# Optimization experiments

Hardware: AMD Instinct MI355X
Metric: run time of the kernel (lower is better)

Reference implementation:

```python
import jax, jax.numpy as jnp
import numpy as np

N = 50000   # nodes
E = 1600000 # edges
NF = 128    # input features
H = 128     # hidden
C = 40      # classes
EPS = 1e-5


def setup_inputs() -> dict:
    key = jax.random.key(0)
    ks = jax.random.split(key, 8)
    s_in = 1.0 / np.sqrt(NF)
    s_h = 1.0 / np.sqrt(H)
    return {
        "x": jax.random.normal(ks[0], (N, NF), jnp.float32),
        "edge_index": jax.random.randint(ks[1], (2, E), 0, N, dtype=jnp.int32),
        "W1": jax.random.normal(ks[2], (NF, H), jnp.float32) * s_in,
        "b1": jnp.zeros((H,), jnp.float32),
        "W2": jax.random.normal(ks[3], (H, H), jnp.float32) * s_h,
        "b2": jnp.zeros((H,), jnp.float32),
        "W3": jax.random.normal(ks[4], (H, H), jnp.float32) * s_h,
        "b3": jnp.zeros((H,), jnp.float32),
        "g1": jnp.ones((H,), jnp.float32), "be1": jnp.zeros((H,), jnp.float32),
        "g2": jnp.ones((H,), jnp.float32), "be2": jnp.zeros((H,), jnp.float32),
        "g3": jnp.ones((H,), jnp.float32), "be3": jnp.zeros((H,), jnp.float32),
        "fcW": jax.random.normal(ks[5], (H, C), jnp.float32) * s_h,
        "fcb": jnp.zeros((C,), jnp.float32),
    }


def _bn(x, g, b):
    # BatchNorm1d training-mode semantics: batch mean / biased batch var
    m = jnp.mean(x, axis=0)
    v = jnp.mean(jnp.square(x - m), axis=0)
    return g * (x - m) * jax.lax.rsqrt(v + EPS) + b


def reference(x, edge_index, W1, b1, W2, b2, W3, b3,
              g1, be1, g2, be2, g3, be3, fcW, fcb):
    n = x.shape[0]
    loop = jnp.arange(n, dtype=edge_index.dtype)
    src = jnp.concatenate([edge_index[0], loop])  # [E+N]
    dst = jnp.concatenate([edge_index[1], loop])
    # symmetric GCN normalization with self-loops
    deg = jax.ops.segment_sum(jnp.ones_like(src, dtype=x.dtype), dst, num_segments=n)
    dis = jnp.where(deg > 0, jax.lax.rsqrt(jnp.maximum(deg, 1.0)), 0.0)
    norm = dis[src] * dis[dst]  # [E+N]

    def conv(h, W, b):
        hw = h @ W  # [n, H]
        msg = hw[src] * norm[:, None]  # [E+N, H] gather + scale
        return jax.ops.segment_sum(msg, dst, num_segments=n) + b  # scatter-add

    h = jax.nn.relu(_bn(conv(x, W1, b1), g1, be1))
    h = jax.nn.relu(_bn(conv(h, W2, b2), g2, be2))  # dropout: eval mode (identity)
    h = jax.nn.relu(_bn(conv(h, W3, b3), g3, be3))
    logits = jax.nn.relu(h @ fcW + fcb)
    return jax.nn.log_softmax(logits, axis=1), logits
```

## Files before the change

kernel.cpp:

```cpp
#include <hip/hip_runtime.h>
#include <hip/hip_bf16.h>
#include <math.h>

#define NODES 50000
#define EDGES 1600000
#define HD    128
#define NC    40
#define EPSV  1e-5f
#define NBKT  196
#define CSRMAX 12032
#define NPART 32

typedef unsigned int uint;
typedef unsigned short ushort;
typedef __attribute__((ext_vector_type(8))) short bfrag;
typedef __attribute__((ext_vector_type(4))) float ffrag;

union FragU { uint4 u; bfrag f; };

__device__ inline ushort bf1(float x) {
  uint u = __float_as_uint(x);
  return (ushort)((u + 0x7fffu + ((u >> 16) & 1u)) >> 16);
}
__device__ inline uint bf2(float a, float b) {
  return (uint)bf1(a) | ((uint)bf1(b) << 16);
}
__device__ inline float ulo(uint u) { return __uint_as_float(u << 16); }
__device__ inline float uhi(uint u) { return __uint_as_float(u & 0xffff0000u); }


__global__ __launch_bounds__(256)
void k_bcount_prepw(const int* __restrict__ dst, int* __restrict__ bcnt, int e_,
                    const float* __restrict__ W1, const float* __restrict__ W2,
                    const float* __restrict__ W3, const float* __restrict__ fcW,
                    ushort* __restrict__ wt) {
  if (blockIdx.x >= 196) {
    int idx = (blockIdx.x - 196) * 256 + threadIdx.x;
    if (idx < 49152) {
      int r = idx >> 14;
      int i = idx & 16383;
      int nn = i >> 7, k = i & 127;
      const float* W = (r == 0) ? W1 : ((r == 1) ? W2 : W3);
      wt[idx] = bf1(W[k * 128 + nn]);
    } else if (idx < 55296) {
      int i = idx - 49152;
      int nn = i >> 7, k = i & 127;
      wt[idx] = (nn < NC) ? bf1(fcW[k * NC + nn]) : (ushort)0;
    }
    return;
  }
  __shared__ int h[256];
  int t = threadIdx.x;
  h[t] = 0;
  __syncthreads();
  int base = blockIdx.x * 8192;
  int cntE = min(8192, e_ - base);
  for (int i = t; i < cntE; i += 256) atomicAdd(&h[dst[base + i] >> 8], 1);
  __syncthreads();
  if (h[t]) atomicAdd(&bcnt[t], h[t]);
}

__global__ void k_bscan(const int* __restrict__ bcnt, int* __restrict__ bbase,
                        int* __restrict__ bcur, int* __restrict__ row_ptr) {
  __shared__ int s[256];
  int t = threadIdx.x;
  int v = bcnt[t];
  s[t] = v;
  __syncthreads();
#pragma unroll
  for (int off = 1; off < 256; off <<= 1) {
    int y = (t >= off) ? s[t - off] : 0;
    __syncthreads();
    s[t] += y;
    __syncthreads();
  }
  int excl = s[t] - v;
  bbase[t] = excl;
  bcur[t] = excl;
  if (t == 255) {
    bbase[256] = s[255];
    row_ptr[NODES] = s[255];
  }
}

__global__ __launch_bounds__(256)
void k_bin(const int* __restrict__ src, const int* __restrict__ dst,
           int* __restrict__ bcur, uint* __restrict__ staging, int e_) {
  __shared__ uint ent[8192];
  __shared__ int h[256], inc[256], lofs[256], cur[256], gb[256];
  int t = threadIdx.x;
  h[t] = 0;
  __syncthreads();
  int base = blockIdx.x * 8192;
  int cntE = min(8192, e_ - base);
  for (int i = t; i < cntE; i += 256) atomicAdd(&h[dst[base + i] >> 8], 1);
  __syncthreads();
  inc[t] = h[t];
  __syncthreads();
#pragma unroll
  for (int off = 1; off < 256; off <<= 1) {
    int y = (t >= off) ? inc[t - off] : 0;
    __syncthreads();
    inc[t] += y;
    __syncthreads();
  }
  lofs[t] = inc[t] - h[t];
  cur[t] = 0;
  __syncthreads();
  for (int i = t; i < cntE; i += 256) {
    int e = base + i;
    int d = dst[e];
    int b = d >> 8;
    uint en = (uint)(src[e] & 0xffff) | ((uint)(d & 255) << 16) | ((uint)b << 24);
    int p = lofs[b] + atomicAdd(&cur[b], 1);
    ent[p] = en;
  }
  __syncthreads();
  if (h[t]) gb[t] = atomicAdd(&bcur[t], h[t]);
  __syncthreads();
  for (int i = t; i < cntE; i += 256) {
    uint en = ent[i];
    int b = en >> 24;
    staging[gb[b] + (i - lofs[b])] = en;
  }
}

__global__ __launch_bounds__(256)
void k_csr(const uint* __restrict__ staging, const int* __restrict__ bbase,
           ushort* __restrict__ csr, int* __restrict__ row_ptr,
           float* __restrict__ dis, int n) {
  __shared__ uint ent[CSRMAX];
  __shared__ ushort srt[CSRMAX];
  __shared__ int cnt_[256], ofs_[256], cur_[256];
  int b = blockIdx.x, t = threadIdx.x;
  int base = bbase[b];
  int cnt = bbase[b + 1] - base;
  if (cnt > CSRMAX) cnt = CSRMAX;
  for (int i = t; i < cnt; i += 256) ent[i] = staging[base + i];
  cnt_[t] = 0;
  __syncthreads();
  for (int i = t; i < cnt; i += 256) atomicAdd(&cnt_[(ent[i] >> 16) & 255], 1);
  __syncthreads();
  ofs_[t] = cnt_[t];
  __syncthreads();
#pragma unroll
  for (int off = 1; off < 256; off <<= 1) {
    int y = (t >= off) ? ofs_[t - off] : 0;
    __syncthreads();
    ofs_[t] += y;
    __syncthreads();
  }
  int myofs = ofs_[t] - cnt_[t];
  ofs_[t] = myofs;
  cur_[t] = 0;
  __syncthreads();
  int node = (b << 8) + t;
  if (node < n) {
    row_ptr[node] = base + myofs;
    dis[node] = rsqrtf((float)(cnt_[t] + 1));
  }
  for (int i = t; i < cnt; i += 256) {
    uint e = ent[i];
    int dl = (e >> 16) & 255;
    int p = ofs_[dl] + atomicAdd(&cur_[dl], 1);
    srt[p] = (ushort)(e & 0xffff);
  }
  __syncthreads();
  for (int i = t; i < cnt; i += 256) csr[base + i] = srt[i];
}

__global__ __launch_bounds__(256)
void k_wfill(const ushort* __restrict__ csr, const int* __restrict__ row_ptr,
             const float* __restrict__ dis, uint* __restrict__ csrw, int n) {
  int node = blockIdx.x * 4 + (threadIdx.x >> 6);
  if (node >= n) return;
  int lane = threadIdx.x & 63;
  int e0 = row_ptr[node], e1 = row_ptr[node + 1];
  float dd = dis[node];
  for (int e = e0 + lane; e < e1; e += 64) {
    int s = csr[e];
    float w = dis[s] * dd;
    csrw[e] = (uint)s | ((uint)bf1(w) << 16);
  }
}

__device__ inline void bn_prologue(const float* __restrict__ part,
                                   const float* __restrict__ g,
                                   const float* __restrict__ be,
                                   float* s_scale, float* s_shift) {
  __shared__ float tmp[256];
  int t = threadIdx.x;
  float s = 0.f;
#pragma unroll 8
  for (int p = 0; p < NPART; ++p) s += part[p * 256 + t];
  tmp[t] = s;
  __syncthreads();
  if (t < 128) {
    const float inv_n = 1.0f / (float)NODES;
    float m = tmp[t] * inv_n;
    float var = tmp[128 + t] * inv_n - m * m;
    float rstd = rsqrtf(var + EPSV);
    float sc = g[t] * rstd;
    s_scale[t] = sc;
    s_shift[t] = be[t] - m * sc;
  }
  __syncthreads();
}

template<int MODE>
__global__ __launch_bounds__(256)
void k_gemm_mx(const void* __restrict__ Ain, const uint* __restrict__ Wt,
               ushort* __restrict__ Cb, int n,
               const float* __restrict__ part, const float* __restrict__ g,
               const float* __restrict__ be) {
  __shared__ float s_scale[128], s_shift[128];
  if (MODE == 1) bn_prologue(part, g, be, s_scale, s_shift);

  const int lane = threadIdx.x & 63;
  const int wave = threadIdx.x >> 6;
  const int quad = lane >> 4;
  const int ml = lane & 15;
  const int row0 = blockIdx.x * 64 + wave * 16;
  const int arow = row0 + ml;
  ffrag acc[8];
#pragma unroll
  for (int i = 0; i < 8; ++i) acc[i] = (ffrag){0.f, 0.f, 0.f, 0.f};

#pragma unroll
  for (int s = 0; s < 4; ++s) {
    const int k0 = s * 32 + quad * 8;
    FragU a;
    if (arow < n) {
      if (MODE == 1) {
        const uint* Ab = (const uint*)Ain;
        uint4 v = *(const uint4*)&Ab[(size_t)arow * 64 + (k0 >> 1)];
        float4 sc0 = *(const float4*)&s_scale[k0];
        float4 sc1 = *(const float4*)&s_scale[k0 + 4];
        float4 sh0 = *(const float4*)&s_shift[k0];
        float4 sh1 = *(const float4*)&s_shift[k0 + 4];
        a.u.x = bf2(fmaxf(fmaf(ulo(v.x), sc0.x, sh0.x), 0.f), fmaxf(fmaf(uhi(v.x), sc0.y, sh0.y), 0.f));
        a.u.y = bf2(fmaxf(fmaf(ulo(v.y), sc0.z, sh0.z), 0.f), fmaxf(fmaf(uhi(v.y), sc0.w, sh0.w), 0.f));
        a.u.z = bf2(fmaxf(fmaf(ulo(v.z), sc1.x, sh1.x), 0.f), fmaxf(fmaf(uhi(v.z), sc1.y, sh1.y), 0.f));
        a.u.w = bf2(fmaxf(fmaf(ulo(v.w), sc1.z, sh1.z), 0.f), fmaxf(fmaf(uhi(v.w), sc1.w, sh1.w), 0.f));
      } else {
        const float* Af = (const float*)Ain;
        float4 a0 = *(const float4*)&Af[(size_t)arow * 128 + k0];
        float4 a1 = *(const float4*)&Af[(size_t)arow * 128 + k0 + 4];
        a.u.x = bf2(a0.x, a0.y);
        a.u.y = bf2(a0.z, a0.w);
        a.u.z = bf2(a1.x, a1.y);
        a.u.w = bf2(a1.z, a1.w);
      }
    } else {
      a.u = make_uint4(0, 0, 0, 0);
    }
#pragma unroll
    for (int nt = 0; nt < 8; ++nt) {
      FragU b;
      b.u = *(const uint4*)&Wt[(size_t)(nt * 16 + ml) * 64 + (k0 >> 1)];
      acc[nt] = __builtin_amdgcn_mfma_f32_16x16x32_bf16(a.f, b.f, acc[nt], 0, 0, 0);
    }
  }
#pragma unroll
  for (int nt = 0; nt < 8; ++nt) {
#pragma unroll
    for (int r = 0; r < 4; ++r) {
      int orow = row0 + quad * 4 + r;
      if (orow < n) Cb[(size_t)orow * 128 + nt * 16 + ml] = bf1(acc[nt][r]);
    }
  }
}

__global__ __launch_bounds__(256)
void k_agg(const uint* __restrict__ t, const int* __restrict__ row_ptr,
           const uint* __restrict__ csrw, const float* __restrict__ dis,
           uint* __restrict__ hb, float* __restrict__ part, int n) {
  __shared__ float redS[4][128], redQ[4][128];
  int lane = threadIdx.x & 63;
  int wave = threadIdx.x >> 6;
  int quarter = lane >> 4;
  int fl = lane & 15;
  int node0 = blockIdx.x * 16 + wave * 4;
  float sS[8] = {}, sQ[8] = {};

  for (int ni = 0; ni < 4; ++ni) {
    int node = node0 + ni;
    int e0 = row_ptr[node], e1 = row_ptr[node + 1];
    float acc[8] = {};
    for (int chunk = e0; chunk < e1; chunk += 64) {
      int m = min(64, e1 - chunk);
      uint ev = 0;
      if (lane < m) ev = csrw[chunk + lane];
#pragma unroll 2
      for (int j = 0; j < m; j += 8) {
        int j0 = j + quarter, j1 = j + 4 + quarter;
        uint ev0 = __shfl(ev, j0, 64);
        uint ev1 = __shfl(ev, j1, 64);
        bool p0 = j0 < m, p1 = j1 < m;
        uint4 v0 = make_uint4(0, 0, 0, 0), v1 = make_uint4(0, 0, 0, 0);
        if (p0) v0 = *(const uint4*)&t[(size_t)(ev0 & 0xffffu) * 64 + (fl << 2)];
        if (p1) v1 = *(const uint4*)&t[(size_t)(ev1 & 0xffffu) * 64 + (fl << 2)];
        float w0 = __uint_as_float(ev0 & 0xffff0000u);
        float w1 = __uint_as_float(ev1 & 0xffff0000u);
        if (p0) {
          acc[0] = fmaf(w0, ulo(v0.x), acc[0]);
          acc[1] = fmaf(w0, uhi(v0.x), acc[1]);
          acc[2] = fmaf(w0, ulo(v0.y), acc[2]);
          acc[3] = fmaf(w0, uhi(v0.y), acc[3]);
          acc[4] = fmaf(w0, ulo(v0.z), acc[4]);
          acc[5] = fmaf(w0, uhi(v0.z), acc[5]);
          acc[6] = fmaf(w0, ulo(v0.w), acc[6]);
          acc[7] = fmaf(w0, uhi(v0.w), acc[7]);
        }
        if (p1) {
          acc[0] = fmaf(w1, ulo(v1.x), acc[0]);
          acc[1] = fmaf(w1, uhi(v1.x), acc[1]);
          acc[2] = fmaf(w1, ulo(v1.y), acc[2]);
          acc[3] = fmaf(w1, uhi(v1.y), acc[3]);
          acc[4] = fmaf(w1, ulo(v1.z), acc[4]);
          acc[5] = fmaf(w1, uhi(v1.z), acc[5]);
          acc[6] = fmaf(w1, ulo(v1.w), acc[6]);
          acc[7] = fmaf(w1, uhi(v1.w), acc[7]);
        }
      }
    }
#pragma unroll
    for (int j = 0; j < 8; ++j) {
      acc[j] += __shfl_xor(acc[j], 16, 64);
      acc[j] += __shfl_xor(acc[j], 32, 64);
    }
    if (quarter == 0) {
      float dd = dis[node];
      float d2 = dd * dd;
      uint4 v = *(const uint4*)&t[(size_t)node * 64 + (fl << 2)];
      acc[0] = fmaf(d2, ulo(v.x), acc[0]);
      acc[1] = fmaf(d2, uhi(v.x), acc[1]);
      acc[2] = fmaf(d2, ulo(v.y), acc[2]);
      acc[3] = fmaf(d2, uhi(v.y), acc[3]);
      acc[4] = fmaf(d2, ulo(v.z), acc[4]);
      acc[5] = fmaf(d2, uhi(v.z), acc[5]);
      acc[6] = fmaf(d2, ulo(v.w), acc[6]);
      acc[7] = fmaf(d2, uhi(v.w), acc[7]);
      uint4 o;
      o.x = bf2(acc[0], acc[1]);
      o.y = bf2(acc[2], acc[3]);
      o.z = bf2(acc[4], acc[5]);
      o.w = bf2(acc[6], acc[7]);
      *(uint4*)&hb[(size_t)node * 64 + (fl << 2)] = o;
#pragma unroll
      for (int j = 0; j < 8; ++j) {
        sS[j] += acc[j];
        sQ[j] += acc[j] * acc[j];
      }
    }
  }
  if (quarter == 0) {
#pragma unroll
    for (int j = 0; j < 8; ++j) {
      redS[wave][fl * 8 + j] = sS[j];
      redQ[wave][fl * 8 + j] = sQ[j];
    }
  }
  __syncthreads();
  int tt = threadIdx.x;
  if (tt < 128) {
    float s = redS[0][tt] + redS[1][tt] + redS[2][tt] + redS[3][tt];
    atomicAdd(&part[(blockIdx.x & (NPART - 1)) * 256 + tt], s);
  } else {
    int f = tt - 128;
    float s = redQ[0][f] + redQ[1][f] + redQ[2][f] + redQ[3][f];
    atomicAdd(&part[(blockIdx.x & (NPART - 1)) * 256 + tt], s);
  }
}

__global__ __launch_bounds__(256)
void k_fc_mx(const uint* __restrict__ hb, const float* __restrict__ part,
             const float* __restrict__ g, const float* __restrict__ be,
             const uint* __restrict__ fWt, const float* __restrict__ fcb,
             float* __restrict__ out, int n) {
  __shared__ float s_scale[128], s_shift[128];
  bn_prologue(part, g, be, s_scale, s_shift);

  const int lane = threadIdx.x & 63;
  const int wave = threadIdx.x >> 6;
  const int quad = lane >> 4;
  const int ml = lane & 15;
  const int row0 = blockIdx.x * 64 + wave * 16;
  const int arow = row0 + ml;
  ffrag acc[3];
#pragma unroll
  for (int i = 0; i < 3; ++i) acc[i] = (ffrag){0.f, 0.f, 0.f, 0.f};

#pragma unroll
  for (int s = 0; s < 4; ++s) {
    const int k0 = s * 32 + quad * 8;
    FragU a;
    if (arow < n) {
      uint4 v = *(const uint4*)&hb[(size_t)arow * 64 + (k0 >> 1)];
      float4 sc0 = *(const float4*)&s_scale[k0];
      float4 sc1 = *(const float4*)&s_scale[k0 + 4];
      float4 sh0 = *(const float4*)&s_shift[k0];
      float4 sh1 = *(const float4*)&s_shift[k0 + 4];
      a.u.x = bf2(fmaxf(fmaf(ulo(v.x), sc0.x, sh0.x), 0.f), fmaxf(fmaf(uhi(v.x), sc0.y, sh0.y), 0.f));
      a.u.y = bf2(fmaxf(fmaf(ulo(v.y), sc0.z, sh0.z), 0.f), fmaxf(fmaf(uhi(v.y), sc0.w, sh0.w), 0.f));
      a.u.z = bf2(fmaxf(fmaf(ulo(v.z), sc1.x, sh1.x), 0.f), fmaxf(fmaf(uhi(v.z), sc1.y, sh1.y), 0.f));
      a.u.w = bf2(fmaxf(fmaf(ulo(v.w), sc1.z, sh1.z), 0.f), fmaxf(fmaf(uhi(v.w), sc1.w, sh1.w), 0.f));
    } else {
      a.u = make_uint4(0, 0, 0, 0);
    }
#pragma unroll
    for (int nt = 0; nt < 3; ++nt) {
      FragU b;
      b.u = *(const uint4*)&fWt[(size_t)(nt * 16 + ml) * 64 + (k0 >> 1)];
      acc[nt] = __builtin_amdgcn_mfma_f32_16x16x32_bf16(a.f, b.f, acc[nt], 0, 0, 0);
    }
  }

  float b0 = fcb[ml], b1 = fcb[16 + ml];
  float b2 = (ml < 8) ? fcb[32 + ml] : 0.f;
#pragma unroll
  for (int r = 0; r < 4; ++r) {
    int orow = row0 + quad * 4 + r;
    if (orow >= n) continue;
    float l0 = fmaxf(acc[0][r] + b0, 0.f);
    float l1 = fmaxf(acc[1][r] + b1, 0.f);
    float l2 = (ml < 8) ? fmaxf(acc[2][r] + b2, 0.f) : -1e30f;
    float mx = fmaxf(fmaxf(l0, l1), l2);
#pragma unroll
    for (int off = 1; off < 16; off <<= 1) mx = fmaxf(mx, __shfl_xor(mx, off, 64));
    float sm = __expf(l0 - mx) + __expf(l1 - mx) + ((ml < 8) ? __expf(l2 - mx) : 0.f);
#pragma unroll
    for (int off = 1; off < 16; off <<= 1) sm += __shfl_xor(sm, off, 64);
    float lse = mx + __logf(sm);
    float* o1 = out + (size_t)orow * NC;
    float* o2 = out + (size_t)NODES * NC + (size_t)orow * NC;
    o1[ml] = l0 - lse;
    o1[16 + ml] = l1 - lse;
    o2[ml] = l0;
    o2[16 + ml] = l1;
    if (ml < 8) {
      o1[32 + ml] = l2 - lse;
      o2[32 + ml] = l2;
    }
  }
}


extern "C" void kernel_launch(void* const* d_in, const int* in_sizes, int n_in,
                              void* d_out, int out_size, void* d_ws, size_t ws_size,
                              hipStream_t stream) {
  (void)in_sizes; (void)n_in; (void)out_size; (void)ws_size;
  const float* x   = (const float*)d_in[0];
  const int*   ei  = (const int*)d_in[1];
  const float* W1  = (const float*)d_in[2];
  const float* W2  = (const float*)d_in[4];
  const float* W3  = (const float*)d_in[6];
  const float* g1  = (const float*)d_in[8];
  const float* be1 = (const float*)d_in[9];
  const float* g2  = (const float*)d_in[10];
  const float* be2 = (const float*)d_in[11];
  const float* g3  = (const float*)d_in[12];
  const float* be3 = (const float*)d_in[13];
  const float* fcW = (const float*)d_in[14];
  const float* fcb = (const float*)d_in[15];
  float* out = (float*)d_out;

  const int n = NODES, e_ = EDGES;
  const int* srcp = ei;
  const int* dstp = ei + e_;

  char* ws = (char*)d_ws;
  size_t off = 0;
  auto alloc = [&](size_t bytes) {
    char* p = ws + off;
    off = (off + bytes + 255) & ~(size_t)255;
    return p;
  };
  float* dis    = (float*)alloc((size_t)n * 4);
  int*   bcnt   = (int*)  alloc(256 * 4);
  float* parts  = (float*)alloc(3 * NPART * 256 * 4);
  int*   bbase  = (int*)  alloc(257 * 4);
  int*   bcur   = (int*)  alloc(256 * 4);
  int*   row_ptr= (int*)  alloc((size_t)(n + 1) * 4);
  uint*  staging= (uint*) alloc((size_t)e_ * 4);
  ushort* csr   = (ushort*)alloc((size_t)e_ * 2);
  uint*  csrw   = (uint*) alloc((size_t)e_ * 4);
  uint*  tbuf   = (uint*) alloc((size_t)n * 64 * 4);
  uint*  hbuf   = (uint*) alloc((size_t)n * 64 * 4);
  ushort* wbuf  = (ushort*)alloc(55296 * 2);

  const uint* Wt1  = (const uint*)wbuf;
  const uint* Wt2  = (const uint*)wbuf + 8192;
  const uint* Wt3  = (const uint*)wbuf + 16384;
  const uint* fWt  = (const uint*)wbuf + 24576;

  const int ebk = (e_ + 8191) / 8192;

  hipMemsetAsync(bcnt, 0, 256 * 4 + 3 * NPART * 256 * 4, stream);
  k_bcount_prepw<<<ebk + 216, 256, 0, stream>>>(dstp, bcnt, e_, W1, W2, W3, fcW, wbuf);
  k_bscan<<<1, 256, 0, stream>>>(bcnt, bbase, bcur, row_ptr);
  k_bin<<<ebk, 256, 0, stream>>>(srcp, dstp, bcur, staging, e_);
  k_csr<<<NBKT, 256, 0, stream>>>(staging, bbase, csr, row_ptr, dis, n);
  k_wfill<<<n / 4, 256, 0, stream>>>(csr, row_ptr, dis, csrw, n);

  const int ggrid = (n + 63) / 64;
  const int agrid = n / 16;
  float* p0 = parts;
  float* p1 = parts + NPART * 256;
  float* p2 = parts + 2 * NPART * 256;

  k_gemm_mx<0><<<ggrid, 256, 0, stream>>>(x, Wt1, (ushort*)tbuf, n, nullptr, nullptr, nullptr);
  k_agg<<<agrid, 256, 0, stream>>>(tbuf, row_ptr, csrw, dis, hbuf, p0, n);
  k_gemm_mx<1><<<ggrid, 256, 0, stream>>>(hbuf, Wt2, (ushort*)tbuf, n, p0, g1, be1);
  k_agg<<<agrid, 256, 0, stream>>>(tbuf, row_ptr, csrw, dis, hbuf, p1, n);
  k_gemm_mx<1><<<ggrid, 256, 0, stream>>>(hbuf, Wt3, (ushort*)tbuf, n, p1, g2, be2);
  k_agg<<<agrid, 256, 0, stream>>>(tbuf, row_ptr, csrw, dis, hbuf, p2, n);
  k_fc_mx<<<ggrid, 256, 0, stream>>>(hbuf, p2, g3, be3, fWt, fcb, out, n);
}
```

Before: 400.8 us.

## Drop bucket count/scan passes using fixed-capacity buckets and fuse edge-weight fill into first aggregation

Removes the bucket-count and scan kernels by giving each destination bucket a fixed CSRMAX-sized slot in staging, with bcur acting as a per-bucket fill counter. Row pointers become (start,end) pairs inside padded buckets. The separate weight-fill kernel is folded into the first aggregation, which computes and stores the packed index/weight pairs for later layers. The gather loop is also unrolled to four edges per step. This cuts launches and a full pass over the edges, at the cost of padded memory and an assumption that no bucket exceeds CSRMAX edges.

```diff
diff --git a/kernel.cpp b/kernel.cpp
--- a/kernel.cpp
+++ b/kernel.cpp
@@ -28,12 +28,12 @@
 __device__ inline float ulo(uint u) { return __uint_as_float(u << 16); }
 __device__ inline float uhi(uint u) { return __uint_as_float(u & 0xffff0000u); }
 
-
 __global__ __launch_bounds__(256)
-void k_bcount_prepw(const int* __restrict__ dst, int* __restrict__ bcnt, int e_,
-                    const float* __restrict__ W1, const float* __restrict__ W2,
-                    const float* __restrict__ W3, const float* __restrict__ fcW,
-                    ushort* __restrict__ wt) {
+void k_bin_prepw(const int* __restrict__ src, const int* __restrict__ dst,
+                 int* __restrict__ bcur, uint* __restrict__ staging, int e_,
+                 const float* __restrict__ W1, const float* __restrict__ W2,
+                 const float* __restrict__ W3, const float* __restrict__ fcW,
+                 ushort* __restrict__ wt) {
   if (blockIdx.x >= 196) {
     int idx = (blockIdx.x - 196) * 256 + threadIdx.x;
     if (idx < 49152) {
@@ -49,43 +49,6 @@
     }
     return;
   }
-  __shared__ int h[256];
-  int t = threadIdx.x;
-  h[t] = 0;
-  __syncthreads();
-  int base = blockIdx.x * 8192;
-  int cntE = min(8192, e_ - base);
-  for (int i = t; i < cntE; i += 256) atomicAdd(&h[dst[base + i] >> 8], 1);
-  __syncthreads();
-  if (h[t]) atomicAdd(&bcnt[t], h[t]);
-}
-
-__global__ void k_bscan(const int* __restrict__ bcnt, int* __restrict__ bbase,
-                        int* __restrict__ bcur, int* __restrict__ row_ptr) {
-  __shared__ int s[256];
-  int t = threadIdx.x;
-  int v = bcnt[t];
-  s[t] = v;
-  __syncthreads();
-#pragma unroll
-  for (int off = 1; off < 256; off <<= 1) {
-    int y = (t >= off) ? s[t - off] : 0;
-    __syncthreads();
-    s[t] += y;
-    __syncthreads();
-  }
-  int excl = s[t] - v;
-  bbase[t] = excl;
-  bcur[t] = excl;
-  if (t == 255) {
-    bbase[256] = s[255];
-    row_ptr[NODES] = s[255];
-  }
-}
-
-__global__ __launch_bounds__(256)
-void k_bin(const int* __restrict__ src, const int* __restrict__ dst,
-           int* __restrict__ bcur, uint* __restrict__ staging, int e_) {
   __shared__ uint ent[8192];
   __shared__ int h[256], inc[256], lofs[256], cur[256], gb[256];
   int t = threadIdx.x;
@@ -121,21 +84,20 @@
   for (int i = t; i < cntE; i += 256) {
     uint en = ent[i];
     int b = en >> 24;
-    staging[gb[b] + (i - lofs[b])] = en;
+    staging[(size_t)b * CSRMAX + gb[b] + (i - lofs[b])] = en;
   }
 }
 
 __global__ __launch_bounds__(256)
-void k_csr(const uint* __restrict__ staging, const int* __restrict__ bbase,
-           ushort* __restrict__ csr, int* __restrict__ row_ptr,
+void k_csr(const uint* __restrict__ staging, const int* __restrict__ bcur,
+           ushort* __restrict__ csr, int2* __restrict__ row_se,
            float* __restrict__ dis, int n) {
   __shared__ uint ent[CSRMAX];
   __shared__ ushort srt[CSRMAX];
   __shared__ int cnt_[256], ofs_[256], cur_[256];
   int b = blockIdx.x, t = threadIdx.x;
-  int base = bbase[b];
-  int cnt = bbase[b + 1] - base;
-  if (cnt > CSRMAX) cnt = CSRMAX;
+  size_t base = (size_t)b * CSRMAX;
+  int cnt = min(bcur[b], CSRMAX);
   for (int i = t; i < cnt; i += 256) ent[i] = staging[base + i];
   cnt_[t] = 0;
   __syncthreads();
@@ -156,7 +118,7 @@
   __syncthreads();
   int node = (b << 8) + t;
   if (node < n) {
-    row_ptr[node] = base + myofs;
+    row_se[node] = make_int2((int)base + myofs, (int)base + myofs + cnt_[t]);
     dis[node] = rsqrtf((float)(cnt_[t] + 1));
   }
   for (int i = t; i < cnt; i += 256) {
@@ -167,21 +129,6 @@
   }
   __syncthreads();
   for (int i = t; i < cnt; i += 256) csr[base + i] = srt[i];
-}
-
-__global__ __launch_bounds__(256)
-void k_wfill(const ushort* __restrict__ csr, const int* __restrict__ row_ptr,
-             const float* __restrict__ dis, uint* __restrict__ csrw, int n) {
-  int node = blockIdx.x * 4 + (threadIdx.x >> 6);
-  if (node >= n) return;
-  int lane = threadIdx.x & 63;
-  int e0 = row_ptr[node], e1 = row_ptr[node + 1];
-  float dd = dis[node];
-  for (int e = e0 + lane; e < e1; e += 64) {
-    int s = csr[e];
-    float w = dis[s] * dd;
-    csrw[e] = (uint)s | ((uint)bf1(w) << 16);
-  }
 }
 
 __device__ inline void bn_prologue(const float* __restrict__ part,
@@ -271,9 +218,11 @@
   }
 }
 
+template<int FIRST>
 __global__ __launch_bounds__(256)
-void k_agg(const uint* __restrict__ t, const int* __restrict__ row_ptr,
-           const uint* __restrict__ csrw, const float* __restrict__ dis,
+void k_agg(const uint* __restrict__ t, const int2* __restrict__ row_se,
+           const ushort* __restrict__ csr, uint* __restrict__ csrw,
+           const float* __restrict__ dis,
            uint* __restrict__ hb, float* __restrict__ part, int n) {
   __shared__ float redS[4][128], redQ[4][128];
   int lane = threadIdx.x & 63;
@@ -285,42 +234,63 @@
 
   for (int ni = 0; ni < 4; ++ni) {
     int node = node0 + ni;
-    int e0 = row_ptr[node], e1 = row_ptr[node + 1];
+    int2 se = row_se[node];
+    int e0 = se.x, e1 = se.y;
+    float dd = dis[node];
     float acc[8] = {};
     for (int chunk = e0; chunk < e1; chunk += 64) {
       int m = min(64, e1 - chunk);
       uint ev = 0;
-      if (lane < m) ev = csrw[chunk + lane];
-#pragma unroll 2
-      for (int j = 0; j < m; j += 8) {
-        int j0 = j + quarter, j1 = j + 4 + quarter;
+      if (lane < m) {
+        if (FIRST) {
+          int s = csr[chunk + lane];
+          float w = dis[s] * dd;
+          ev = (uint)s | ((uint)bf1(w) << 16);
+          csrw[chunk + lane] = ev;
+        } else {
+          ev = csrw[chunk + lane];
+        }
+      }
+      for (int j = 0; j < m; j += 16) {
+        int j0 = j + quarter, j1 = j + 4 + quarter, j2 = j + 8 + quarter, j3 = j + 12 + quarter;
         uint ev0 = __shfl(ev, j0, 64);
         uint ev1 = __shfl(ev, j1, 64);
-        bool p0 = j0 < m, p1 = j1 < m;
-        uint4 v0 = make_uint4(0, 0, 0, 0), v1 = make_uint4(0, 0, 0, 0);
+        uint ev2 = __shfl(ev, j2, 64);
+        uint ev3 = __shfl(ev, j3, 64);
+        bool p0 = j0 < m, p1 = j1 < m, p2 = j2 < m, p3 = j3 < m;
+        uint4 v0 = make_uint4(0,0,0,0), v1 = make_uint4(0,0,0,0);
+        uint4 v2 = make_uint4(0,0,0,0), v3 = make_uint4(0,0,0,0);
         if (p0) v0 = *(const uint4*)&t[(size_t)(ev0 & 0xffffu) * 64 + (fl << 2)];
         if (p1) v1 = *(const uint4*)&t[(size_t)(ev1 & 0xffffu) * 64 + (fl << 2)];
+        if (p2) v2 = *(const uint4*)&t[(size_t)(ev2 & 0xffffu) * 64 + (fl << 2)];
+        if (p3) v3 = *(const uint4*)&t[(size_t)(ev3 & 0xffffu) * 64 + (fl << 2)];
         float w0 = __uint_as_float(ev0 & 0xffff0000u);
         float w1 = __uint_as_float(ev1 & 0xffff0000u);
+        float w2 = __uint_as_float(ev2 & 0xffff0000u);
+        float w3 = __uint_as_float(ev3 & 0xffff0000u);
         if (p0) {
-          acc[0] = fmaf(w0, ulo(v0.x), acc[0]);
-          acc[1] = fmaf(w0, uhi(v0.x), acc[1]);
-          acc[2] = fmaf(w0, ulo(v0.y), acc[2]);
-          acc[3] = fmaf(w0, uhi(v0.y), acc[3]);
-          acc[4] = fmaf(w0, ulo(v0.z), acc[4]);
-          acc[5] = fmaf(w0, uhi(v0.z), acc[5]);
-          acc[6] = fmaf(w0, ulo(v0.w), acc[6]);
-          acc[7] = fmaf(w0, uhi(v0.w), acc[7]);
+          acc[0] = fmaf(w0, ulo(v0.x), acc[0]); acc[1] = fmaf(w0, uhi(v0.x), acc[1]);
+          acc[2] = fmaf(w0, ulo(v0.y), acc[2]); acc[3] = fmaf(w0, uhi(v0.y), acc[3]);
+          acc[4] = fmaf(w0, ulo(v0.z), acc[4]); acc[5] = fmaf(w0, uhi(v0.z), acc[5]);
+          acc[6] = fmaf(w0, ulo(v0.w), acc[6]); acc[7] = fmaf(w0, uhi(v0.w), acc[7]);
         }
         if (p1) {
-          acc[0] = fmaf(w1, ulo(v1.x), acc[0]);
-          acc[1] = fmaf(w1, uhi(v1.x), acc[1]);
-          acc[2] = fmaf(w1, ulo(v1.y), acc[2]);
-          acc[3] = fmaf(w1, uhi(v1.y), acc[3]);
-          acc[4] = fmaf(w1, ulo(v1.z), acc[4]);
-          acc[5] = fmaf(w1, uhi(v1.z), acc[5]);
-          acc[6] = fmaf(w1, ulo(v1.w), acc[6]);
-          acc[7] = fmaf(w1, uhi(v1.w), acc[7]);
+          acc[0] = fmaf(w1, ulo(v1.x), acc[0]); acc[1] = fmaf(w1, uhi(v1.x), acc[1]);
+          acc[2] = fmaf(w1, ulo(v1.y), acc[2]); acc[3] = fmaf(w1, uhi(v1.y), acc[3]);
+          acc[4] = fmaf(w1, ulo(v1.z), acc[4]); acc[5] = fmaf(w1, uhi(v1.z), acc[5]);
+          acc[6] = fmaf(w1, ulo(v1.w), acc[6]); acc[7] = fmaf(w1, uhi(v1.w), acc[7]);
+        }
+        if (p2) {
+          acc[0] = fmaf(w2, ulo(v2.x), acc[0]); acc[1] = fmaf(w2, uhi(v2.x), acc[1]);
+          acc[2] = fmaf(w2, ulo(v2.y), acc[2]); acc[3] = fmaf(w2, uhi(v2.y), acc[3]);
+          acc[4] = fmaf(w2, ulo(v2.z), acc[4]); acc[5] = fmaf(w2, uhi(v2.z), acc[5]);
+          acc[6] = fmaf(w2, ulo(v2.w), acc[6]); acc[7] = fmaf(w2, uhi(v2.w), acc[7]);
+        }
+        if (p3) {
+          acc[0] = fmaf(w3, ulo(v3.x), acc[0]); acc[1] = fmaf(w3, uhi(v3.x), acc[1]);
+          acc[2] = fmaf(w3, ulo(v3.y), acc[2]); acc[3] = fmaf(w3, uhi(v3.y), acc[3]);
+          acc[4] = fmaf(w3, ulo(v3.z), acc[4]); acc[5] = fmaf(w3, uhi(v3.z), acc[5]);
+          acc[6] = fmaf(w3, ulo(v3.w), acc[6]); acc[7] = fmaf(w3, uhi(v3.w), acc[7]);
         }
       }
     }
@@ -330,17 +300,12 @@
       acc[j] += __shfl_xor(acc[j], 32, 64);
     }
     if (quarter == 0) {
-      float dd = dis[node];
       float d2 = dd * dd;
       uint4 v = *(const uint4*)&t[(size_t)node * 64 + (fl << 2)];
-      acc[0] = fmaf(d2, ulo(v.x), acc[0]);
-      acc[1] = fmaf(d2, uhi(v.x), acc[1]);
-      acc[2] = fmaf(d2, ulo(v.y), acc[2]);
-      acc[3] = fmaf(d2, uhi(v.y), acc[3]);
-      acc[4] = fmaf(d2, ulo(v.z), acc[4]);
-      acc[5] = fmaf(d2, uhi(v.z), acc[5]);
-      acc[6] = fmaf(d2, ulo(v.w), acc[6]);
-      acc[7] = fmaf(d2, uhi(v.w), acc[7]);
+      acc[0] = fmaf(d2, ulo(v.x), acc[0]); acc[1] = fmaf(d2, uhi(v.x), acc[1]);
+      acc[2] = fmaf(d2, ulo(v.y), acc[2]); acc[3] = fmaf(d2, uhi(v.y), acc[3]);
+      acc[4] = fmaf(d2, ulo(v.z), acc[4]); acc[5] = fmaf(d2, uhi(v.z), acc[5]);
+      acc[6] = fmaf(d2, ulo(v.w), acc[6]); acc[7] = fmaf(d2, uhi(v.w), acc[7]);
       uint4 o;
       o.x = bf2(acc[0], acc[1]);
       o.y = bf2(acc[2], acc[3]);
@@ -477,14 +442,12 @@
     return p;
   };
   float* dis    = (float*)alloc((size_t)n * 4);
-  int*   bcnt   = (int*)  alloc(256 * 4);
+  int*   bcur   = (int*)  alloc(256 * 4);
   float* parts  = (float*)alloc(3 * NPART * 256 * 4);
-  int*   bbase  = (int*)  alloc(257 * 4);
-  int*   bcur   = (int*)  alloc(256 * 4);
-  int*   row_ptr= (int*)  alloc((size_t)(n + 1) * 4);
-  uint*  staging= (uint*) alloc((size_t)e_ * 4);
-  ushort* csr   = (ushort*)alloc((size_t)e_ * 2);
-  uint*  csrw   = (uint*) alloc((size_t)e_ * 4);
+  int2*  row_se = (int2*) alloc((size_t)n * 8);
+  uint*  staging= (uint*) alloc((size_t)NBKT * CSRMAX * 4);
+  ushort* csr   = (ushort*)alloc((size_t)NBKT * CSRMAX * 2);
+  uint*  csrw   = (uint*) alloc((size_t)NBKT * CSRMAX * 4);
   uint*  tbuf   = (uint*) alloc((size_t)n * 64 * 4);
   uint*  hbuf   = (uint*) alloc((size_t)n * 64 * 4);
   ushort* wbuf  = (ushort*)alloc(55296 * 2);
@@ -494,14 +457,10 @@
   const uint* Wt3  = (const uint*)wbuf + 16384;
   const uint* fWt  = (const uint*)wbuf + 24576;
 
-  const int ebk = (e_ + 8191) / 8192;
-
-  hipMemsetAsync(bcnt, 0, 256 * 4 + 3 * NPART * 256 * 4, stream);
-  k_bcount_prepw<<<ebk + 216, 256, 0, stream>>>(dstp, bcnt, e_, W1, W2, W3, fcW, wbuf);
-  k_bscan<<<1, 256, 0, stream>>>(bcnt, bbase, bcur, row_ptr);
-  k_bin<<<ebk, 256, 0, stream>>>(srcp, dstp, bcur, staging, e_);
-  k_csr<<<NBKT, 256, 0, stream>>>(staging, bbase, csr, row_ptr, dis, n);
-  k_wfill<<<n / 4, 256, 0, stream>>>(csr, row_ptr, dis, csrw, n);
+  hipMemsetAsync(bcur, 0, 256 * 4 + 3 * NPART * 256 * 4, stream);
+  k_bin_prepw<<<196 + 216, 256, 0, stream>>>(srcp, dstp, bcur, staging, e_,
+                                             W1, W2, W3, fcW, wbuf);
+  k_csr<<<NBKT, 256, 0, stream>>>(staging, bcur, csr, row_se, dis, n);
 
   const int ggrid = (n + 63) / 64;
   const int agrid = n / 16;
@@ -510,10 +469,10 @@
   float* p2 = parts + 2 * NPART * 256;
 
   k_gemm_mx<0><<<ggrid, 256, 0, stream>>>(x, Wt1, (ushort*)tbuf, n, nullptr, nullptr, nullptr);
-  k_agg<<<agrid, 256, 0, stream>>>(tbuf, row_ptr, csrw, dis, hbuf, p0, n);
+  k_agg<1><<<agrid, 256, 0, stream>>>(tbuf, row_se, csr, csrw, dis, hbuf, p0, n);
   k_gemm_mx<1><<<ggrid, 256, 0, stream>>>(hbuf, Wt2, (ushort*)tbuf, n, p0, g1, be1);
-  k_agg<<<agrid, 256, 0, stream>>>(tbuf, row_ptr, csrw, dis, hbuf, p1, n);
+  k_agg<0><<<agrid, 256, 0, stream>>>(tbuf, row_se, csr, csrw, dis, hbuf, p1, n);
   k_gemm_mx<1><<<ggrid, 256, 0, stream>>>(hbuf, Wt3, (ushort*)tbuf, n, p1, g2, be2);
-  k_agg<<<agrid, 256, 0, stream>>>(tbuf, row_ptr, csrw, dis, hbuf, p2, n);
+  k_agg<0><<<agrid, 256, 0, stream>>>(tbuf, row_se, csr, csrw, dis, hbuf, p2, n);
   k_fc_mx<<<ggrid, 256, 0, stream>>>(hbuf, p2, g3, be3, fWt, fcb, out, n);
 }
```

Result: faster. 379.5 us (-5.3%).
